# Performance work log

Hardware: AMD Instinct MI355X
Metric: run time of the kernel (lower is better)

The kernel has to match this reference:

```python
import jax, jax.numpy as jnp
import numpy as np

BN_EPS = 1e-5

def setup_inputs() -> dict:
    key = jax.random.key(0)
    k1, k2, k3 = jax.random.split(key, 3)
    B, D_IN, D_OUT = 16384, 2048, 1024
    stdv = np.sqrt(1.5 / (D_IN + D_OUT))
    x = jax.random.normal(k1, (B, D_IN), dtype=jnp.float32)
    weight = jax.random.uniform(k2, (D_OUT, D_IN), dtype=jnp.float32, minval=-stdv, maxval=stdv)
    bias = jax.random.normal(k3, (D_OUT,), dtype=jnp.float32) * 0.01
    gamma = jnp.ones((D_OUT,), dtype=jnp.float32)
    beta = jnp.zeros((D_OUT,), dtype=jnp.float32)
    return {"x": x, "weight": weight, "bias": bias, "gamma": gamma, "beta": beta}

def reference(x, weight, bias, gamma, beta):
    # STE-binarized weights: forward uses sign(w) (>=0 -> +1), grad flows via clamp(w,-1,1)
    w_sign = jnp.where(weight >= 0, 1.0, -1.0).astype(weight.dtype)
    w_clip = jnp.clip(weight, -1.0, 1.0)
    w_bin = jax.lax.stop_gradient(w_sign - w_clip) + w_clip
    # y = x @ w_bin.T + bias   -> [B, D_OUT]
    y = jnp.einsum('bi,oi->bo', x, w_bin) + bias[None, :]
    # BatchNorm1d (training mode: batch statistics, biased variance)
    mean = jnp.mean(y, axis=0)
    var = jnp.mean((y - mean) ** 2, axis=0)
    y_norm = (y - mean) * jax.lax.rsqrt(var + BN_EPS)
    return y_norm * gamma + beta
```

## Files before the change

### kernel.cpp

```cpp
#include <hip/hip_runtime.h>
#include <hip/hip_bf16.h>

typedef __attribute__((ext_vector_type(4))) float f32x4;
typedef __attribute__((ext_vector_type(8))) __bf16 bf16x8;
typedef __attribute__((ext_vector_type(4))) unsigned int uint4v;

constexpr int M = 16384;
constexpr int N = 1024;
constexpr int K = 2048;
constexpr int BM = 256, BN = 256, BK = 64;
constexpr int NKT = K / BK;
constexpr float BN_EPS = 1e-5f;
constexpr int TM2 = M / BM;

#define GLOAD_LDS16(g, l)                                                      \
  __builtin_amdgcn_global_load_lds(                                            \
      (const __attribute__((address_space(1))) void*)(g),                      \
      (__attribute__((address_space(3))) void*)(l), 16, 0, 0)

#define SB0 __builtin_amdgcn_sched_barrier(0)
#define BARRIER __builtin_amdgcn_s_barrier()
#define LGKM0 asm volatile("s_waitcnt lgkmcnt(0)" ::: "memory")
#define VMC(n) asm volatile("s_waitcnt vmcnt(" #n ")" ::: "memory")

__device__ __forceinline__ unsigned sgnbf(float f) {
  return (f >= 0.f) ? 0x3F80u : 0xBF80u;
}
__global__ __launch_bounds__(256) void binw_kernel(
    const float* __restrict__ w, uint4v* __restrict__ wb) {
  size_t i = (size_t)blockIdx.x * 256 + threadIdx.x;
  const f32x4* win = (const f32x4*)w;
  f32x4 v0 = win[i * 2];
  f32x4 v1 = win[i * 2 + 1];
  uint4v o;
  o.x = sgnbf(v0[0]) | (sgnbf(v0[1]) << 16);
  o.y = sgnbf(v0[2]) | (sgnbf(v0[3]) << 16);
  o.z = sgnbf(v1[0]) | (sgnbf(v1[1]) << 16);
  o.w = sgnbf(v1[2]) | (sgnbf(v1[3]) << 16);
  wb[i] = o;
}

__global__ __launch_bounds__(512, 2) void gemm_bin_kernel(
    const float* __restrict__ Af, const unsigned short* __restrict__ B,
    float* __restrict__ Y, float* __restrict__ psum, float* __restrict__ psq) {
  __shared__ unsigned short Asd[2][2][8192];
  __shared__ unsigned short Bsd[2][2][8192];
  __shared__ float redsum[2][256];
  __shared__ float redsq[2][256];

  const int tid = threadIdx.x;
  const int wid = tid >> 6;
  const int lane = tid & 63;
  const int wr = wid >> 2, wc = wid & 3;

  const int bid = blockIdx.x;
  const int swz = (bid & 7) * 32 + (bid >> 3);
  const int tm = swz >> 2, tn = swz & 3;
  const size_t m0 = (size_t)tm * BM, n0 = (size_t)tn * BN;

  const int frow = lane & 15;
  const int fcb = lane >> 4;
  const int swq = (frow >> 1) & 3;
  const int aoff = (wr * 128 + frow) * 32 + (fcb ^ swq) * 8;
  const int boff = (wc * 64 + frow) * 32 + (fcb ^ swq) * 8;

  const unsigned short* pBg =
      B + (n0 + wid * 32 + (lane >> 2)) * (size_t)K +
      (((lane & 3) ^ ((lane >> 3) & 3)) * 8);

  const size_t aRowK = (m0 + wid * 32 + (lane >> 2)) * (size_t)K;
  const float* pAg = Af + aRowK + (((lane & 3) ^ ((lane >> 3) & 3)) * 8);
  const int awb = (wid * 32 + (lane >> 2)) * 32 + (lane & 3) * 8;

  f32x4 acc[8][4];
#pragma unroll
  for (int mi = 0; mi < 8; ++mi)
#pragma unroll
    for (int nj = 0; nj < 4; ++nj)
#pragma unroll
      for (int j = 0; j < 4; ++j) acc[mi][nj][j] = 0.f;

  f32x4 xq0, xq1, xq2, xq3, xq4, xq5, xq6, xq7;

#define BG(g, ks, t, NS)                                                       \
  GLOAD_LDS16(pBg + (size_t)(g)*16 * K + (size_t)(t)*64 + (ks)*32,             \
              &Bsd[NS][ks][(wid * 32 + (g)*16) * 32])

#define ALOAD(t)                                                               \
  {                                                                            \
    const float* p_ = pAg + (size_t)(t)*64;                                    \
    xq0 = *(const f32x4*)(p_);                                                 \
    xq1 = *(const f32x4*)(p_ + 4);                                             \
    xq2 = *(const f32x4*)(p_ + 16 * (size_t)K);                                \
    xq3 = *(const f32x4*)(p_ + 16 * (size_t)K + 4);                            \
    xq4 = *(const f32x4*)(p_ + 32);                                            \
    xq5 = *(const f32x4*)(p_ + 36);                                            \
    xq6 = *(const f32x4*)(p_ + 16 * (size_t)K + 32);                           \
    xq7 = *(const f32x4*)(p_ + 16 * (size_t)K + 36);                           \
  }
#define CVW(dst, ra, rb)                                                       \
  {                                                                            \
    bf16x8 v_;                                                                 \
    _Pragma("unroll") for (int j_ = 0; j_ < 4; ++j_) {                         \
      v_[j_] = (__bf16)(ra)[j_];                                               \
      v_[4 + j_] = (__bf16)(rb)[j_];                                           \
    }                                                                          \
    *(bf16x8*)(dst) = v_;                                                      \
  }
#define AWRITE(NS)                                                             \
  {                                                                            \
    CVW(&Asd[NS][0][awb], xq0, xq1);                                           \
    CVW(&Asd[NS][0][awb + 512], xq2, xq3);                                     \
    CVW(&Asd[NS][1][awb], xq4, xq5);                                           \
    CVW(&Asd[NS][1][awb + 512], xq6, xq7);                                     \
  }

#define MQ(MB)                                                                 \
  LGKM0;                                                                       \
  SB0;                                                                         \
  __builtin_amdgcn_s_setprio(1);                                               \
  _Pragma("unroll") for (int i_ = 0; i_ < 4; ++i_)                             \
      _Pragma("unroll") for (int j_ = 0; j_ < 4; ++j_) acc[(MB) + i_][j_] =    \
          __builtin_amdgcn_mfma_f32_16x16x32_bf16(aq[i_], bq[j_],              \
                                                  acc[(MB) + i_][j_], 0, 0,    \
                                                  0);                          \
  __builtin_amdgcn_s_setprio(0);                                               \
  SB0;

#define TILE(S, NS, t, STG)                                                    \
  {                                                                            \
    bf16x8 aq[4], bq[4];                                                       \
                           \
    _Pragma("unroll") for (int j_ = 0; j_ < 4; ++j_) bq[j_] =                  \
        *(const bf16x8*)&Bsd[S][0][boff + j_ * 512];                           \
    _Pragma("unroll") for (int i_ = 0; i_ < 4; ++i_) aq[i_] =                  \
        *(const bf16x8*)&Asd[S][0][aoff + i_ * 512];                           \
    SB0;                                                                       \
    if (STG) {                                                                 \
      BG(0, 0, (t) + 1, NS);                                                   \
      BG(1, 0, (t) + 1, NS);                                                   \
      SB0;                                                                     \
    }                                                                          \
    BARRIER;                                                                   \
    MQ(0);                                                                     \
    BARRIER;                                                                   \
           \
    _Pragma("unroll") for (int i_ = 0; i_ < 4; ++i_) aq[i_] =                  \
        *(const bf16x8*)&Asd[S][0][aoff + (4 + i_) * 512];                     \
    SB0;                                                                       \
    if (STG) {                                                                 \
      BG(0, 1, (t) + 1, NS);                                                   \
      BG(1, 1, (t) + 1, NS);                                                   \
      SB0;                                                                     \
      ALOAD((t) + 1);                                                          \
      SB0;                                                                     \
    }                                                                          \
    BARRIER;                                                                   \
    MQ(4);                                                                     \
    BARRIER;                                                                   \
                                                 \
    _Pragma("unroll") for (int j_ = 0; j_ < 4; ++j_) bq[j_] =                  \
        *(const bf16x8*)&Bsd[S][1][boff + j_ * 512];                           \
    _Pragma("unroll") for (int i_ = 0; i_ < 4; ++i_) aq[i_] =                  \
        *(const bf16x8*)&Asd[S][1][aoff + i_ * 512];                           \
    SB0;                                                                       \
    BARRIER;                                                                   \
    MQ(0);                                                                     \
    BARRIER;                                                                   \
        \
          \
    _Pragma("unroll") for (int i_ = 0; i_ < 4; ++i_) aq[i_] =                  \
        *(const bf16x8*)&Asd[S][1][aoff + (4 + i_) * 512];                     \
    SB0;                                                                       \
    if (STG) {                                                                 \
      AWRITE(NS);                                                              \
      SB0;                                                                     \
    }                                                                          \
    BARRIER;                                                                   \
    MQ(4);                                                                     \
    if (STG) BARRIER;                                                          \
  }

  BG(0, 0, 0, 0);
  BG(1, 0, 0, 0);
  BG(0, 1, 0, 0);
  BG(1, 1, 0, 0);
  SB0;
  ALOAD(0);
  SB0;
  AWRITE(0);
  LGKM0;
  BARRIER;

  for (int t = 0; t < NKT - 2; t += 2) {
    TILE(0, 1, t, 1);
    TILE(1, 0, t + 1, 1);
  }
  TILE(0, 1, NKT - 2, 1);
  TILE(1, 0, NKT - 1, 0);

#pragma unroll
  for (int nj = 0; nj < 4; ++nj) {
    float s = 0.f, q = 0.f;
#pragma unroll
    for (int mi = 0; mi < 8; ++mi)
#pragma unroll
      for (int j = 0; j < 4; ++j) {
        float v = acc[mi][nj][j];
        s += v;
        q += v * v;
      }
    s += __shfl_xor(s, 16);
    s += __shfl_xor(s, 32);
    q += __shfl_xor(q, 16);
    q += __shfl_xor(q, 32);
    if (fcb == 0) {
      redsum[wr][wc * 64 + nj * 16 + frow] = s;
      redsq[wr][wc * 64 + nj * 16 + frow] = q;
    }
  }
  __syncthreads();
  if (tid < BN) {
    psum[(size_t)tm * N + n0 + tid] = redsum[0][tid] + redsum[1][tid];
    psq[(size_t)tm * N + n0 + tid] = redsq[0][tid] + redsq[1][tid];
  }

#pragma unroll
  for (int mi = 0; mi < 8; ++mi) {
    const size_t r0 = m0 + wr * 128 + mi * 16 + fcb * 4;
#pragma unroll
    for (int nj = 0; nj < 4; ++nj) {
      float* yp = Y + r0 * N + n0 + wc * 64 + nj * 16 + frow;
#pragma unroll
      for (int j = 0; j < 4; ++j) yp[(size_t)j * N] = acc[mi][nj][j];
    }
  }
}

__global__ __launch_bounds__(256) void bnstats_kernel(
    const float* __restrict__ psum, const float* __restrict__ psq,
    const float* __restrict__ gamma, const float* __restrict__ beta,
    float* __restrict__ scale, float* __restrict__ shift) {
  const int c = blockIdx.x * 256 + threadIdx.x;
  float s = 0.f, q = 0.f;
  for (int i = 0; i < TM2; ++i) {
    s += psum[i * N + c];
    q += psq[i * N + c];
  }
  const float mean = s * (1.f / (float)M);
  const float var = q * (1.f / (float)M) - mean * mean;
  const float inv = rsqrtf(var + BN_EPS);
  const float sc = gamma[c] * inv;
  scale[c] = sc;
  shift[c] = beta[c] - mean * sc;
}

__global__ __launch_bounds__(256) void bnapply_kernel(
    float* __restrict__ Y, const float* __restrict__ scale,
    const float* __restrict__ shift) {
  const size_t i = (size_t)blockIdx.x * 256 + threadIdx.x;
  f32x4 y = ((const f32x4*)Y)[i];
  const int c = (int)((i * 4) & (N - 1));
  f32x4 sc = *(const f32x4*)&scale[c];
  f32x4 sh = *(const f32x4*)&shift[c];
  ((f32x4*)Y)[i] = y * sc + sh;
}

extern "C" void kernel_launch(void* const* d_in, const int* in_sizes, int n_in,
                              void* d_out, int out_size, void* d_ws,
                              size_t ws_size, hipStream_t stream) {
  const float* x = (const float*)d_in[0];
  const float* w = (const float*)d_in[1];
  const float* gamma = (const float*)d_in[3];
  const float* beta = (const float*)d_in[4];
  float* Y = (float*)d_out;

  char* ws = (char*)d_ws;
  uint4v* wb = (uint4v*)ws;
  float* psum = (float*)(ws + (size_t)N * K * 2);
  float* psq = psum + (size_t)TM2 * N;
  float* scale = psq + (size_t)TM2 * N;
  float* shift = scale + N;

  binw_kernel<<<(N * K / 8) / 256, 256, 0, stream>>>(w, wb);
  gemm_bin_kernel<<<(M / BM) * (N / BN), 512, 0, stream>>>(
      x, (const unsigned short*)wb, Y, psum, psq);
  bnstats_kernel<<<N / 256, 256, 0, stream>>>(psum, psq, gamma, beta, scale,
                                              shift);
  bnapply_kernel<<<(M * N / 4) / 256, 256, 0, stream>>>(Y, scale, shift);
}
```

Measured before the change: 116.8 us.

## Pre-cast x to bf16 and stream both GEMM operands via direct-to-LDS loads

Adds a separate kernel that converts x from fp32 to bf16 into workspace. The GEMM then fetches both A and B with global_load_lds DMA instead of register loads plus in-loop conversion and LDS writes. This cuts register pressure and VALU/LDS-write work inside the main loop. In exchange it adds an extra pass that reads 128MB and writes 64MB, plus a full vmcnt wait per tile. A fallback to the old kernel runs if the workspace is too small.

```diff
diff --git a/kernel.cpp b/kernel.cpp
--- a/kernel.cpp
+++ b/kernel.cpp
@@ -40,8 +40,22 @@
   wb[i] = o;
 }
 
-__global__ __launch_bounds__(512, 2) void gemm_bin_kernel(
-    const float* __restrict__ Af, const unsigned short* __restrict__ B,
+__global__ __launch_bounds__(256) void castx_kernel(
+    const float* __restrict__ x, unsigned short* __restrict__ xb) {
+  const size_t i = ((size_t)blockIdx.x * 256 + threadIdx.x) * 8;
+  f32x4 a = *(const f32x4*)(x + i);
+  f32x4 b = *(const f32x4*)(x + i + 4);
+  bf16x8 v;
+#pragma unroll
+  for (int j = 0; j < 4; ++j) {
+    v[j] = (__bf16)a[j];
+    v[4 + j] = (__bf16)b[j];
+  }
+  *(bf16x8*)(xb + i) = v;
+}
+
+__global__ __launch_bounds__(512, 2) void gemm_dma_kernel(
+    const unsigned short* __restrict__ Axb, const unsigned short* __restrict__ B,
     float* __restrict__ Y, float* __restrict__ psum, float* __restrict__ psq) {
   __shared__ unsigned short Asd[2][2][8192];
   __shared__ unsigned short Bsd[2][2][8192];
@@ -64,13 +78,10 @@
   const int aoff = (wr * 128 + frow) * 32 + (fcb ^ swq) * 8;
   const int boff = (wc * 64 + frow) * 32 + (fcb ^ swq) * 8;
 
-  const unsigned short* pBg =
-      B + (n0 + wid * 32 + (lane >> 2)) * (size_t)K +
-      (((lane & 3) ^ ((lane >> 3) & 3)) * 8);
-
-  const size_t aRowK = (m0 + wid * 32 + (lane >> 2)) * (size_t)K;
-  const float* pAg = Af + aRowK + (((lane & 3) ^ ((lane >> 3) & 3)) * 8);
-  const int awb = (wid * 32 + (lane >> 2)) * 32 + (lane & 3) * 8;
+  const int gch = ((lane & 3) ^ ((lane >> 3) & 3)) * 8;
+  const int grow = wid * 32 + (lane >> 2);
+  const unsigned short* pAx = Axb + (m0 + grow) * (size_t)K + gch;
+  const unsigned short* pBx = B + (n0 + grow) * (size_t)K + gch;
 
   f32x4 acc[8][4];
 #pragma unroll
@@ -80,40 +91,12 @@
 #pragma unroll
       for (int j = 0; j < 4; ++j) acc[mi][nj][j] = 0.f;
 
-  f32x4 xq0, xq1, xq2, xq3, xq4, xq5, xq6, xq7;
-
-#define BG(g, ks, t, NS)                                                       \
-  GLOAD_LDS16(pBg + (size_t)(g)*16 * K + (size_t)(t)*64 + (ks)*32,             \
+#define ADMA(g, ks, t, NS)                                                     \
+  GLOAD_LDS16(pAx + (size_t)(g)*16 * K + (size_t)(t)*64 + (ks)*32,             \
+              &Asd[NS][ks][(wid * 32 + (g)*16) * 32])
+#define BDMA(g, ks, t, NS)                                                     \
+  GLOAD_LDS16(pBx + (size_t)(g)*16 * K + (size_t)(t)*64 + (ks)*32,             \
               &Bsd[NS][ks][(wid * 32 + (g)*16) * 32])
-
-#define ALOAD(t)                                                               \
-  {                                                                            \
-    const float* p_ = pAg + (size_t)(t)*64;                                    \
-    xq0 = *(const f32x4*)(p_);                                                 \
-    xq1 = *(const f32x4*)(p_ + 4);                                             \
-    xq2 = *(const f32x4*)(p_ + 16 * (size_t)K);                                \
-    xq3 = *(const f32x4*)(p_ + 16 * (size_t)K + 4);                            \
-    xq4 = *(const f32x4*)(p_ + 32);                                            \
-    xq5 = *(const f32x4*)(p_ + 36);                                            \
-    xq6 = *(const f32x4*)(p_ + 16 * (size_t)K + 32);                           \
-    xq7 = *(const f32x4*)(p_ + 16 * (size_t)K + 36);                           \
-  }
-#define CVW(dst, ra, rb)                                                       \
-  {                                                                            \
-    bf16x8 v_;                                                                 \
-    _Pragma("unroll") for (int j_ = 0; j_ < 4; ++j_) {                         \
-      v_[j_] = (__bf16)(ra)[j_];                                               \
-      v_[4 + j_] = (__bf16)(rb)[j_];                                           \
-    }                                                                          \
-    *(bf16x8*)(dst) = v_;                                                      \
-  }
-#define AWRITE(NS)                                                             \
-  {                                                                            \
-    CVW(&Asd[NS][0][awb], xq0, xq1);                                           \
-    CVW(&Asd[NS][0][awb + 512], xq2, xq3);                                     \
-    CVW(&Asd[NS][1][awb], xq4, xq5);                                           \
-    CVW(&Asd[NS][1][awb + 512], xq6, xq7);                                     \
-  }
 
 #define MQ(MB)                                                                 \
   LGKM0;                                                                       \
@@ -130,29 +113,31 @@
 #define TILE(S, NS, t, STG)                                                    \
   {                                                                            \
     bf16x8 aq[4], bq[4];                                                       \
-                           \
+                         \
     _Pragma("unroll") for (int j_ = 0; j_ < 4; ++j_) bq[j_] =                  \
         *(const bf16x8*)&Bsd[S][0][boff + j_ * 512];                           \
     _Pragma("unroll") for (int i_ = 0; i_ < 4; ++i_) aq[i_] =                  \
         *(const bf16x8*)&Asd[S][0][aoff + i_ * 512];                           \
     SB0;                                                                       \
     if (STG) {                                                                 \
-      BG(0, 0, (t) + 1, NS);                                                   \
-      BG(1, 0, (t) + 1, NS);                                                   \
+      ADMA(0, 0, (t) + 1, NS);                                                 \
+      ADMA(1, 0, (t) + 1, NS);                                                 \
+      BDMA(0, 0, (t) + 1, NS);                                                 \
+      BDMA(1, 0, (t) + 1, NS);                                                 \
       SB0;                                                                     \
     }                                                                          \
     BARRIER;                                                                   \
     MQ(0);                                                                     \
     BARRIER;                                                                   \
-           \
+                     \
     _Pragma("unroll") for (int i_ = 0; i_ < 4; ++i_) aq[i_] =                  \
         *(const bf16x8*)&Asd[S][0][aoff + (4 + i_) * 512];                     \
     SB0;                                                                       \
     if (STG) {                                                                 \
-      BG(0, 1, (t) + 1, NS);                                                   \
-      BG(1, 1, (t) + 1, NS);                                                   \
-      SB0;                                                                     \
-      ALOAD((t) + 1);                                                          \
+      ADMA(0, 1, (t) + 1, NS);                                                 \
+      ADMA(1, 1, (t) + 1, NS);                                                 \
+      BDMA(0, 1, (t) + 1, NS);                                                 \
+      BDMA(1, 1, (t) + 1, NS);                                                 \
       SB0;                                                                     \
     }                                                                          \
     BARRIER;                                                                   \
@@ -168,28 +153,27 @@
     MQ(0);                                                                     \
     BARRIER;                                                                   \
         \
-          \
     _Pragma("unroll") for (int i_ = 0; i_ < 4; ++i_) aq[i_] =                  \
         *(const bf16x8*)&Asd[S][1][aoff + (4 + i_) * 512];                     \
     SB0;                                                                       \
-    if (STG) {                                                                 \
-      AWRITE(NS);                                                              \
-      SB0;                                                                     \
-    }                                                                          \
     BARRIER;                                                                   \
     MQ(4);                                                                     \
-    if (STG) BARRIER;                                                          \
-  }
-
-  BG(0, 0, 0, 0);
-  BG(1, 0, 0, 0);
-  BG(0, 1, 0, 0);
-  BG(1, 1, 0, 0);
+    if (STG) {                                                                 \
+      VMC(0);                                                                  \
+      BARRIER;                                                                 \
+    }                                                                          \
+  }
+
+  ADMA(0, 0, 0, 0);
+  ADMA(1, 0, 0, 0);
+  BDMA(0, 0, 0, 0);
+  BDMA(1, 0, 0, 0);
+  ADMA(0, 1, 0, 0);
+  ADMA(1, 1, 0, 0);
+  BDMA(0, 1, 0, 0);
+  BDMA(1, 1, 0, 0);
   SB0;
-  ALOAD(0);
-  SB0;
-  AWRITE(0);
-  LGKM0;
+  VMC(0);
   BARRIER;
 
   for (int t = 0; t < NKT - 2; t += 2) {
@@ -198,6 +182,11 @@
   }
   TILE(0, 1, NKT - 2, 1);
   TILE(1, 0, NKT - 1, 0);
+
+#undef ADMA
+#undef BDMA
+#undef MQ
+#undef TILE
 
 #pragma unroll
   for (int nj = 0; nj < 4; ++nj) {
@@ -237,6 +226,200 @@
   }
 }
 
+__global__ __launch_bounds__(512, 2) void gemm_fb_kernel(
+    const float* __restrict__ Af, const unsigned short* __restrict__ B,
+    float* __restrict__ Y, float* __restrict__ psum, float* __restrict__ psq) {
+  __shared__ unsigned short Asd[2][2][8192];
+  __shared__ unsigned short Bsd[2][2][8192];
+  __shared__ float redsum[2][256];
+  __shared__ float redsq[2][256];
+
+  const int tid = threadIdx.x;
+  const int wid = tid >> 6;
+  const int lane = tid & 63;
+  const int wr = wid >> 2, wc = wid & 3;
+
+  const int bid = blockIdx.x;
+  const int swz = (bid & 7) * 32 + (bid >> 3);
+  const int tm = swz >> 2, tn = swz & 3;
+  const size_t m0 = (size_t)tm * BM, n0 = (size_t)tn * BN;
+
+  const int frow = lane & 15;
+  const int fcb = lane >> 4;
+  const int swq = (frow >> 1) & 3;
+  const int aoff = (wr * 128 + frow) * 32 + (fcb ^ swq) * 8;
+  const int boff = (wc * 64 + frow) * 32 + (fcb ^ swq) * 8;
+
+  const unsigned short* pBg = B + (n0 + wid * 32 + (lane >> 2)) * (size_t)K +
+                              (((lane & 3) ^ ((lane >> 3) & 3)) * 8);
+  const size_t aRowK = (m0 + wid * 32 + (lane >> 2)) * (size_t)K;
+  const float* pAg = Af + aRowK + (((lane & 3) ^ ((lane >> 3) & 3)) * 8);
+  const int awb = (wid * 32 + (lane >> 2)) * 32 + (lane & 3) * 8;
+
+  f32x4 acc[8][4];
+#pragma unroll
+  for (int mi = 0; mi < 8; ++mi)
+#pragma unroll
+    for (int nj = 0; nj < 4; ++nj)
+#pragma unroll
+      for (int j = 0; j < 4; ++j) acc[mi][nj][j] = 0.f;
+
+  f32x4 xq0, xq1, xq2, xq3, xq4, xq5, xq6, xq7;
+
+#define BG(g, ks, t, NS)                                                       \
+  GLOAD_LDS16(pBg + (size_t)(g)*16 * K + (size_t)(t)*64 + (ks)*32,             \
+              &Bsd[NS][ks][(wid * 32 + (g)*16) * 32])
+#define ALOAD(t)                                                               \
+  {                                                                            \
+    const float* p_ = pAg + (size_t)(t)*64;                                    \
+    xq0 = *(const f32x4*)(p_);                                                 \
+    xq1 = *(const f32x4*)(p_ + 4);                                             \
+    xq2 = *(const f32x4*)(p_ + 16 * (size_t)K);                                \
+    xq3 = *(const f32x4*)(p_ + 16 * (size_t)K + 4);                            \
+    xq4 = *(const f32x4*)(p_ + 32);                                            \
+    xq5 = *(const f32x4*)(p_ + 36);                                            \
+    xq6 = *(const f32x4*)(p_ + 16 * (size_t)K + 32);                           \
+    xq7 = *(const f32x4*)(p_ + 16 * (size_t)K + 36);                           \
+  }
+#define CVW(dst, ra, rb)                                                       \
+  {                                                                            \
+    bf16x8 v_;                                                                 \
+    _Pragma("unroll") for (int j_ = 0; j_ < 4; ++j_) {                         \
+      v_[j_] = (__bf16)(ra)[j_];                                               \
+      v_[4 + j_] = (__bf16)(rb)[j_];                                           \
+    }                                                                          \
+    *(bf16x8*)(dst) = v_;                                                      \
+  }
+#define AWRITE(NS)                                                             \
+  {                                                                            \
+    CVW(&Asd[NS][0][awb], xq0, xq1);                                           \
+    CVW(&Asd[NS][0][awb + 512], xq2, xq3);                                     \
+    CVW(&Asd[NS][1][awb], xq4, xq5);                                           \
+    CVW(&Asd[NS][1][awb + 512], xq6, xq7);                                     \
+  }
+#define MQ(MB)                                                                 \
+  LGKM0;                                                                       \
+  SB0;                                                                         \
+  __builtin_amdgcn_s_setprio(1);                                               \
+  _Pragma("unroll") for (int i_ = 0; i_ < 4; ++i_)                             \
+      _Pragma("unroll") for (int j_ = 0; j_ < 4; ++j_) acc[(MB) + i_][j_] =    \
+          __builtin_amdgcn_mfma_f32_16x16x32_bf16(aq[i_], bq[j_],              \
+                                                  acc[(MB) + i_][j_], 0, 0,    \
+                                                  0);                          \
+  __builtin_amdgcn_s_setprio(0);                                               \
+  SB0;
+
+#define TILE(S, NS, t, STG)                                                    \
+  {                                                                            \
+    bf16x8 aq[4], bq[4];                                                       \
+    _Pragma("unroll") for (int j_ = 0; j_ < 4; ++j_) bq[j_] =                  \
+        *(const bf16x8*)&Bsd[S][0][boff + j_ * 512];                           \
+    _Pragma("unroll") for (int i_ = 0; i_ < 4; ++i_) aq[i_] =                  \
+        *(const bf16x8*)&Asd[S][0][aoff + i_ * 512];                           \
+    SB0;                                                                       \
+    if (STG) {                                                                 \
+      BG(0, 0, (t) + 1, NS);                                                   \
+      BG(1, 0, (t) + 1, NS);                                                   \
+      SB0;                                                                     \
+    }                                                                          \
+    BARRIER;                                                                   \
+    MQ(0);                                                                     \
+    BARRIER;                                                                   \
+    _Pragma("unroll") for (int i_ = 0; i_ < 4; ++i_) aq[i_] =                  \
+        *(const bf16x8*)&Asd[S][0][aoff + (4 + i_) * 512];                     \
+    SB0;                                                                       \
+    if (STG) {                                                                 \
+      BG(0, 1, (t) + 1, NS);                                                   \
+      BG(1, 1, (t) + 1, NS);                                                   \
+      SB0;                                                                     \
+      ALOAD((t) + 1);                                                          \
+      SB0;                                                                     \
+    }                                                                          \
+    BARRIER;                                                                   \
+    MQ(4);                                                                     \
+    BARRIER;                                                                   \
+    _Pragma("unroll") for (int j_ = 0; j_ < 4; ++j_) bq[j_] =                  \
+        *(const bf16x8*)&Bsd[S][1][boff + j_ * 512];                           \
+    _Pragma("unroll") for (int i_ = 0; i_ < 4; ++i_) aq[i_] =                  \
+        *(const bf16x8*)&Asd[S][1][aoff + i_ * 512];                           \
+    SB0;                                                                       \
+    BARRIER;                                                                   \
+    MQ(0);                                                                     \
+    BARRIER;                                                                   \
+    _Pragma("unroll") for (int i_ = 0; i_ < 4; ++i_) aq[i_] =                  \
+        *(const bf16x8*)&Asd[S][1][aoff + (4 + i_) * 512];                     \
+    SB0;                                                                       \
+    if (STG) {                                                                 \
+      AWRITE(NS);                                                              \
+      SB0;                                                                     \
+    }                                                                          \
+    BARRIER;                                                                   \
+    MQ(4);                                                                     \
+    if (STG) BARRIER;                                                          \
+  }
+
+  BG(0, 0, 0, 0);
+  BG(1, 0, 0, 0);
+  BG(0, 1, 0, 0);
+  BG(1, 1, 0, 0);
+  SB0;
+  ALOAD(0);
+  SB0;
+  AWRITE(0);
+  LGKM0;
+  BARRIER;
+
+  for (int t = 0; t < NKT - 2; t += 2) {
+    TILE(0, 1, t, 1);
+    TILE(1, 0, t + 1, 1);
+  }
+  TILE(0, 1, NKT - 2, 1);
+  TILE(1, 0, NKT - 1, 0);
+
+#undef BG
+#undef ALOAD
+#undef CVW
+#undef AWRITE
+#undef MQ
+#undef TILE
+
+#pragma unroll
+  for (int nj = 0; nj < 4; ++nj) {
+    float s = 0.f, q = 0.f;
+#pragma unroll
+    for (int mi = 0; mi < 8; ++mi)
+#pragma unroll
+      for (int j = 0; j < 4; ++j) {
+        float v = acc[mi][nj][j];
+        s += v;
+        q += v * v;
+      }
+    s += __shfl_xor(s, 16);
+    s += __shfl_xor(s, 32);
+    q += __shfl_xor(q, 16);
+    q += __shfl_xor(q, 32);
+    if (fcb == 0) {
+      redsum[wr][wc * 64 + nj * 16 + frow] = s;
+      redsq[wr][wc * 64 + nj * 16 + frow] = q;
+    }
+  }
+  __syncthreads();
+  if (tid < BN) {
+    psum[(size_t)tm * N + n0 + tid] = redsum[0][tid] + redsum[1][tid];
+    psq[(size_t)tm * N + n0 + tid] = redsq[0][tid] + redsq[1][tid];
+  }
+#pragma unroll
+  for (int mi = 0; mi < 8; ++mi) {
+    const size_t r0 = m0 + wr * 128 + mi * 16 + fcb * 4;
+#pragma unroll
+    for (int nj = 0; nj < 4; ++nj) {
+      float* yp = Y + r0 * N + n0 + wc * 64 + nj * 16 + frow;
+#pragma unroll
+      for (int j = 0; j < 4; ++j) yp[(size_t)j * N] = acc[mi][nj][j];
+    }
+  }
+}
+
 __global__ __launch_bounds__(256) void bnstats_kernel(
     const float* __restrict__ psum, const float* __restrict__ psq,
     const float* __restrict__ gamma, const float* __restrict__ beta,
@@ -277,14 +460,23 @@
 
   char* ws = (char*)d_ws;
   uint4v* wb = (uint4v*)ws;
-  float* psum = (float*)(ws + (size_t)N * K * 2);
+  float* psum = (float*)(ws + ((size_t)4 << 20));
   float* psq = psum + (size_t)TM2 * N;
   float* scale = psq + (size_t)TM2 * N;
   float* shift = scale + N;
+  unsigned short* xb = (unsigned short*)(ws + ((size_t)8 << 20));
+  const size_t need = ((size_t)8 << 20) + (size_t)M * K * 2;
 
   binw_kernel<<<(N * K / 8) / 256, 256, 0, stream>>>(w, wb);
-  gemm_bin_kernel<<<(M / BM) * (N / BN), 512, 0, stream>>>(
-      x, (const unsigned short*)wb, Y, psum, psq);
+
+  if (ws_size >= need) {
+    castx_kernel<<<(int)(((size_t)M * K / 8) / 256), 256, 0, stream>>>(x, xb);
+    gemm_dma_kernel<<<(M / BM) * (N / BN), 512, 0, stream>>>(
+        xb, (const unsigned short*)wb, Y, psum, psq);
+  } else {
+    gemm_fb_kernel<<<(M / BM) * (N / BN), 512, 0, stream>>>(
+        x, (const unsigned short*)wb, Y, psum, psq);
+  }
   bnstats_kernel<<<N / 256, 256, 0, stream>>>(psum, psq, gamma, beta, scale,
                                               shift);
   bnapply_kernel<<<(M * N / 4) / 256, 256, 0, stream>>>(Y, scale, shift);
```

Result: slower. 133.7 us (+14.5%).
